# Optimization experiments

Hardware: AMD Instinct MI355X
Metric: run time of the kernel (lower is better)

The kernel has to match this reference:

```python
import jax, jax.numpy as jnp
import numpy as np

BN_EPS = 1e-5

def setup_inputs() -> dict:
    key = jax.random.key(0)
    k1, k2, k3, k4 = jax.random.split(key, 4)
    B, V, DI, DO = 4096, 64, 128, 128
    feat = jax.random.normal(k1, (B, V, DI), dtype=jnp.float32)
    adj = jax.random.uniform(k2, (V, V), dtype=jnp.float32)
    # per-vertex Linear weights (stacked): W[v] maps dim_in -> dim_out
    W = jax.random.normal(k3, (V, DI, DO), dtype=jnp.float32) * (1.0 / np.sqrt(DI))
    b = jax.random.normal(k4, (V, DO), dtype=jnp.float32) * 0.01
    gamma = jnp.ones((V, DO), dtype=jnp.float32)
    beta = jnp.zeros((V, DO), dtype=jnp.float32)
    return {"feat": feat, "adj": adj, "W": W, "b": b, "gamma": gamma, "beta": beta}

def reference(feat, adj, W, b, gamma, beta):
    # Per-vertex Linear as one grouped GEMM: [B,V,DI] x [V,DI,DO] -> [B,V,DO]
    h = jnp.einsum('bvi,vio->bvo', feat, W) + b[None, :, :]
    # BatchNorm1d (training mode): normalize over batch dim, per vertex & channel
    mu = jnp.mean(h, axis=0, keepdims=True)            # [1,V,DO]
    var = jnp.mean((h - mu) ** 2, axis=0, keepdims=True)  # biased variance
    h = (h - mu) * jax.lax.rsqrt(var + BN_EPS) * gamma[None] + beta[None]
    # adjacency mix: adj [V,V] applied to every batch element, then relu
    out = jnp.einsum('uv,bvo->buo', adj, h)
    return jax.nn.relu(out)
```

## Files before the change

### kernel.cpp

```cpp
#include <hip/hip_runtime.h>

#define BN 4096
#define VN 64
#define DI 128
#define DO 128

typedef __attribute__((ext_vector_type(8))) short short8;
typedef __attribute__((ext_vector_type(4))) float f32x4;

__device__ __forceinline__ float bf2f(unsigned short s) {
    return __uint_as_float(((unsigned)s) << 16);
}
__device__ __forceinline__ unsigned short f2bf(float f) {
    unsigned u = __float_as_uint(f);
    u += 0x7FFF + ((u >> 16) & 1);
    return (unsigned short)(u >> 16);
}
__device__ __forceinline__ unsigned pack_bf16_trunc(float lo, float hi) {
    return __builtin_amdgcn_perm(__float_as_uint(hi), __float_as_uint(lo), 0x07060302u);
}

__global__ __launch_bounds__(256) void k_prep(const float* __restrict__ W,
                                              const float* __restrict__ adj,
                                              unsigned short* __restrict__ Wt,
                                              unsigned short* __restrict__ adjbf,
                                              float* __restrict__ stats) {
    const int t = threadIdx.x, blk = blockIdx.x;
    if (blk < 256) {
        const int v = blk >> 2, q = blk & 3;
        const float* Wv = W + (size_t)v * DI * DO;
        unsigned short* Wtv = Wt + (size_t)v * DI * DO;
        const int o = t & 127;
        const int i0 = q * 32 + (t >> 7) * 16;
        short8 s0, s1;
#pragma unroll
        for (int j = 0; j < 8; ++j)
            s0[j] = (short)f2bf(Wv[(size_t)(i0 + j) * DO + o]);
#pragma unroll
        for (int j = 0; j < 8; ++j)
            s1[j] = (short)f2bf(Wv[(size_t)(i0 + 8 + j) * DO + o]);
        *(short8*)(Wtv + o * DI + i0) = s0;
        *(short8*)(Wtv + o * DI + i0 + 8) = s1;
    } else if (blk == 256) {
        short8 s0, s1;
#pragma unroll
        for (int j = 0; j < 8; ++j) s0[j] = (short)f2bf(adj[t * 16 + j]);
#pragma unroll
        for (int j = 0; j < 8; ++j) s1[j] = (short)f2bf(adj[t * 16 + 8 + j]);
        *(short8*)(adjbf + t * 16) = s0;
        *(short8*)(adjbf + t * 16 + 8) = s1;
    } else {
        const f32x4 z = {0.f, 0.f, 0.f, 0.f};
#pragma unroll
        for (int k = 0; k < 16; ++k)
            *(f32x4*)(stats + (size_t)(k * 256 + t) * 4) = z;
    }
}

__global__ __launch_bounds__(256) void k_gemm1(const float* __restrict__ feat,
                                               const unsigned short* __restrict__ Wt,
                                               const float* __restrict__ bias,
                                               unsigned short* __restrict__ h,
                                               float* __restrict__ sum_,
                                               float* __restrict__ sumsq_) {
    const int bt = blockIdx.x;
    const int v = blockIdx.y;
    const int tid = threadIdx.x;
    const int w = tid >> 6, lane = tid & 63;
    const int wm = w >> 1, wn = w & 1;
    const int quad = lane >> 4, l16 = lane & 15;

    size_t aidx[4];
    const unsigned short* Bbase[4];
#pragma unroll
    for (int rt = 0; rt < 4; ++rt)
        aidx[rt] = (size_t)(bt * 128 + wm * 64 + rt * 16 + l16) * (VN * DI)
                 + v * DI + quad * 8;
#pragma unroll
    for (int nt = 0; nt < 4; ++nt)
        Bbase[nt] = Wt + (size_t)v * (DI * DO)
                       + (size_t)(wn * 64 + nt * 16 + l16) * DI + quad * 8;

    f32x4 acc[4][4];
#pragma unroll
    for (int rt = 0; rt < 4; ++rt)
#pragma unroll
        for (int nt = 0; nt < 4; ++nt) acc[rt][nt] = (f32x4){0.f, 0.f, 0.f, 0.f};

#pragma unroll
    for (int k0 = 0; k0 < DI; k0 += 32) {
        short8 a[4], bb[4];
#pragma unroll
        for (int rt = 0; rt < 4; ++rt) {
            f32x4 f0 = *(const f32x4*)(feat + aidx[rt] + k0);
            f32x4 f1 = *(const f32x4*)(feat + aidx[rt] + k0 + 4);
            union { short8 s; unsigned u[4]; } pk;
            pk.u[0] = pack_bf16_trunc(f0[0], f0[1]);
            pk.u[1] = pack_bf16_trunc(f0[2], f0[3]);
            pk.u[2] = pack_bf16_trunc(f1[0], f1[1]);
            pk.u[3] = pack_bf16_trunc(f1[2], f1[3]);
            a[rt] = pk.s;
        }
#pragma unroll
        for (int nt = 0; nt < 4; ++nt) bb[nt] = *(const short8*)(Bbase[nt] + k0);
#pragma unroll
        for (int rt = 0; rt < 4; ++rt)
#pragma unroll
            for (int nt = 0; nt < 4; ++nt)
                acc[rt][nt] = __builtin_amdgcn_mfma_f32_16x16x32_bf16(
                    a[rt], bb[nt], acc[rt][nt], 0, 0, 0);
    }

#pragma unroll
    for (int nt = 0; nt < 4; ++nt) {
        const int col = wn * 64 + nt * 16 + l16;
        const float bv = bias[v * DO + col];
        float s = 0.f, sq = 0.f;
#pragma unroll
        for (int rt = 0; rt < 4; ++rt)
#pragma unroll
            for (int e = 0; e < 4; ++e) {
                float x = acc[rt][nt][e] + bv;
                acc[rt][nt][e] = x;
                s += x;
                sq += x * x;
            }
        s += __shfl_down(s, 32);  s += __shfl_down(s, 16);
        sq += __shfl_down(sq, 32); sq += __shfl_down(sq, 16);
        if (lane < 16) {
            atomicAdd(&sum_[v * DO + col], s);
            atomicAdd(&sumsq_[v * DO + col], sq);
        }
#pragma unroll
        for (int rt = 0; rt < 4; ++rt)
#pragma unroll
            for (int e = 0; e < 4; ++e) {
                int brow = bt * 128 + wm * 64 + rt * 16 + quad * 4 + e;
                h[(size_t)brow * (VN * DO) + v * DO + col] = f2bf(acc[rt][nt][e]);
            }
    }
}

__global__ __launch_bounds__(128) void k_stats(const float* __restrict__ sum_,
                                               const float* __restrict__ sumsq_,
                                               const float* __restrict__ adj,
                                               const float* __restrict__ gamma,
                                               const float* __restrict__ beta,
                                               float* __restrict__ scale,
                                               float* __restrict__ C0) {
    const int o = threadIdx.x;
    const int u = blockIdx.x;
    const float invB = 1.0f / (float)BN;
    if (u < VN) {
        float c0 = 0.f;
#pragma unroll
        for (int v = 0; v < VN; ++v) {
            float mu = sum_[v * DO + o] * invB;
            float var = sumsq_[v * DO + o] * invB - mu * mu;
            float inv = rsqrtf(var + 1e-5f);
            float sc = gamma[v * DO + o] * inv;
            c0 += adj[u * VN + v] * (beta[v * DO + o] - mu * sc);
        }
        C0[u * DO + o] = c0;
    } else {
#pragma unroll
        for (int v = 0; v < VN; ++v) {
            float mu = sum_[v * DO + o] * invB;
            float var = sumsq_[v * DO + o] * invB - mu * mu;
            scale[v * DO + o] = gamma[v * DO + o] * rsqrtf(var + 1e-5f);
        }
    }
}

__global__ __launch_bounds__(256) void k_mix(const unsigned short* __restrict__ h,
                                             const float* __restrict__ scale,
                                             const unsigned short* __restrict__ adjbf,
                                             const float* __restrict__ C0,
                                             float* __restrict__ out) {
    __shared__ unsigned short hsT[2][DO][72];
    const int t = threadIdx.x;
    const int b0 = blockIdx.x * 2;

    const int sv = t & 63;
#pragma unroll
    for (int c = 0; c < 8; ++c) {
        const int bl = c >> 2;
        const int o0 = ((t >> 6) << 3) + (c & 3) * 32;
        short8 hv = *(const short8*)(h + ((size_t)(b0 + bl) * VN + sv) * DO + o0);
        f32x4 s0 = *(const f32x4*)(scale + sv * DO + o0);
        f32x4 s1 = *(const f32x4*)(scale + sv * DO + o0 + 4);
#pragma unroll
        for (int j = 0; j < 4; ++j)
            hsT[bl][o0 + j][sv] = f2bf(bf2f((unsigned short)hv[j]) * s0[j]);
#pragma unroll
        for (int j = 0; j < 4; ++j)
            hsT[bl][o0 + 4 + j][sv] = f2bf(bf2f((unsigned short)hv[4 + j]) * s1[j]);
    }
    __syncthreads();

    const int w = t >> 6, lane = t & 63;
    const int bl = w >> 1, nh = w & 1;
    const int quad = lane >> 4, l16 = lane & 15;
    const int b = b0 + bl;

    short8 af[4][2];
#pragma unroll
    for (int mt = 0; mt < 4; ++mt)
#pragma unroll
        for (int ks = 0; ks < 2; ++ks)
            af[mt][ks] = *(const short8*)(adjbf + (mt * 16 + l16) * VN
                                          + ks * 32 + quad * 8);

    f32x4 acc[4][4];
#pragma unroll
    for (int mt = 0; mt < 4; ++mt)
#pragma unroll
        for (int nt = 0; nt < 4; ++nt) acc[mt][nt] = (f32x4){0.f, 0.f, 0.f, 0.f};

#pragma unroll
    for (int nt = 0; nt < 4; ++nt) {
        const unsigned short* bp = &hsT[bl][nh * 64 + nt * 16 + l16][quad * 8];
        short8 bf0 = *(const short8*)(bp);
        short8 bf1 = *(const short8*)(bp + 32);
#pragma unroll
        for (int mt = 0; mt < 4; ++mt) {
            acc[mt][nt] = __builtin_amdgcn_mfma_f32_16x16x32_bf16(
                af[mt][0], bf0, acc[mt][nt], 0, 0, 0);
            acc[mt][nt] = __builtin_amdgcn_mfma_f32_16x16x32_bf16(
                af[mt][1], bf1, acc[mt][nt], 0, 0, 0);
        }
    }

#pragma unroll
    for (int mt = 0; mt < 4; ++mt)
#pragma unroll
        for (int nt = 0; nt < 4; ++nt) {
            const int o = nh * 64 + nt * 16 + l16;
#pragma unroll
            for (int e = 0; e < 4; ++e) {
                const int u = mt * 16 + quad * 4 + e;
                out[((size_t)b * VN + u) * DO + o] =
                    fmaxf(acc[mt][nt][e] + C0[u * DO + o], 0.0f);
            }
        }
}

extern "C" void kernel_launch(void* const* d_in, const int* in_sizes, int n_in,
                              void* d_out, int out_size, void* d_ws, size_t ws_size,
                              hipStream_t stream) {
    const float* feat  = (const float*)d_in[0];
    const float* adj   = (const float*)d_in[1];
    const float* W     = (const float*)d_in[2];
    const float* bias  = (const float*)d_in[3];
    const float* gamma = (const float*)d_in[4];
    const float* beta  = (const float*)d_in[5];
    float* out = (float*)d_out;

    char* ws = (char*)d_ws;
    unsigned short* h     = (unsigned short*)ws;
    unsigned short* Wt    = (unsigned short*)(ws + 67108864ull);
    unsigned short* adjbf = (unsigned short*)(ws + 69206016ull);
    float* sum_   = (float*)(ws + 69214208ull);
    float* sumsq_ = sum_ + 8192;
    float* scale  = sumsq_ + 8192;
    float* C0     = scale + 8192;

    k_prep<<<dim3(258), dim3(256), 0, stream>>>(W, adj, Wt, adjbf, sum_);
    k_gemm1<<<dim3(32, 64), dim3(256), 0, stream>>>(feat, Wt, bias, h, sum_, sumsq_);
    k_stats<<<dim3(65), dim3(128), 0, stream>>>(sum_, sumsq_, adj, gamma, beta, scale, C0);
    k_mix<<<dim3(2048), dim3(256), 0, stream>>>(h, scale, adjbf, C0, out);
}
```

Baseline: 339.8 us.

## Replace BN stat atomics with partial sums, prefetch A tiles, preload W

BatchNorm sum and sum-of-squares atomics in the GEMM are replaced by per-block partial sums written to workspace. A new reduce kernel folds them into scale and shift, and a separate kernel computes the adjacency-mixed C0, so the stats zeroing pass is no longer needed. The GEMM now loads all W fragments into registers up front and double-buffers the feature loads across k-steps to overlap memory with MFMA. The prep kernel splits the W transpose across twice as many blocks. In exchange there is one extra kernel launch, and register pressure in the GEMM rises, which may lower occupancy.

```diff
diff --git a/kernel.cpp b/kernel.cpp
--- a/kernel.cpp
+++ b/kernel.cpp
@@ -23,25 +23,20 @@
 __global__ __launch_bounds__(256) void k_prep(const float* __restrict__ W,
                                               const float* __restrict__ adj,
                                               unsigned short* __restrict__ Wt,
-                                              unsigned short* __restrict__ adjbf,
-                                              float* __restrict__ stats) {
+                                              unsigned short* __restrict__ adjbf) {
     const int t = threadIdx.x, blk = blockIdx.x;
-    if (blk < 256) {
-        const int v = blk >> 2, q = blk & 3;
+    if (blk < 512) {
+        const int v = blk >> 3, q = blk & 7;
         const float* Wv = W + (size_t)v * DI * DO;
         unsigned short* Wtv = Wt + (size_t)v * DI * DO;
         const int o = t & 127;
-        const int i0 = q * 32 + (t >> 7) * 16;
-        short8 s0, s1;
+        const int i0 = q * 16 + (t >> 7) * 8;
+        short8 s0;
 #pragma unroll
         for (int j = 0; j < 8; ++j)
             s0[j] = (short)f2bf(Wv[(size_t)(i0 + j) * DO + o]);
-#pragma unroll
-        for (int j = 0; j < 8; ++j)
-            s1[j] = (short)f2bf(Wv[(size_t)(i0 + 8 + j) * DO + o]);
         *(short8*)(Wtv + o * DI + i0) = s0;
-        *(short8*)(Wtv + o * DI + i0 + 8) = s1;
-    } else if (blk == 256) {
+    } else {
         short8 s0, s1;
 #pragma unroll
         for (int j = 0; j < 8; ++j) s0[j] = (short)f2bf(adj[t * 16 + j]);
@@ -49,11 +44,6 @@
         for (int j = 0; j < 8; ++j) s1[j] = (short)f2bf(adj[t * 16 + 8 + j]);
         *(short8*)(adjbf + t * 16) = s0;
         *(short8*)(adjbf + t * 16 + 8) = s1;
-    } else {
-        const f32x4 z = {0.f, 0.f, 0.f, 0.f};
-#pragma unroll
-        for (int k = 0; k < 16; ++k)
-            *(f32x4*)(stats + (size_t)(k * 256 + t) * 4) = z;
     }
 }
 
@@ -61,8 +51,8 @@
                                                const unsigned short* __restrict__ Wt,
                                                const float* __restrict__ bias,
                                                unsigned short* __restrict__ h,
-                                               float* __restrict__ sum_,
-                                               float* __restrict__ sumsq_) {
+                                               float* __restrict__ psA,
+                                               float* __restrict__ psB) {
     const int bt = blockIdx.x;
     const int v = blockIdx.y;
     const int tid = threadIdx.x;
@@ -71,15 +61,19 @@
     const int quad = lane >> 4, l16 = lane & 15;
 
     size_t aidx[4];
-    const unsigned short* Bbase[4];
 #pragma unroll
     for (int rt = 0; rt < 4; ++rt)
         aidx[rt] = (size_t)(bt * 128 + wm * 64 + rt * 16 + l16) * (VN * DI)
                  + v * DI + quad * 8;
-#pragma unroll
-    for (int nt = 0; nt < 4; ++nt)
-        Bbase[nt] = Wt + (size_t)v * (DI * DO)
-                       + (size_t)(wn * 64 + nt * 16 + l16) * DI + quad * 8;
+
+    short8 bb[4][4];
+#pragma unroll
+    for (int ks = 0; ks < 4; ++ks)
+#pragma unroll
+        for (int nt = 0; nt < 4; ++nt)
+            bb[ks][nt] = *(const short8*)(Wt + (size_t)v * (DI * DO)
+                                          + (size_t)(wn * 64 + nt * 16 + l16) * DI
+                                          + quad * 8 + ks * 32);
 
     f32x4 acc[4][4];
 #pragma unroll
@@ -87,29 +81,35 @@
 #pragma unroll
         for (int nt = 0; nt < 4; ++nt) acc[rt][nt] = (f32x4){0.f, 0.f, 0.f, 0.f};
 
-#pragma unroll
-    for (int k0 = 0; k0 < DI; k0 += 32) {
-        short8 a[4], bb[4];
-#pragma unroll
-        for (int rt = 0; rt < 4; ++rt) {
-            f32x4 f0 = *(const f32x4*)(feat + aidx[rt] + k0);
-            f32x4 f1 = *(const f32x4*)(feat + aidx[rt] + k0 + 4);
-            union { short8 s; unsigned u[4]; } pk;
-            pk.u[0] = pack_bf16_trunc(f0[0], f0[1]);
-            pk.u[1] = pack_bf16_trunc(f0[2], f0[3]);
-            pk.u[2] = pack_bf16_trunc(f1[0], f1[1]);
-            pk.u[3] = pack_bf16_trunc(f1[2], f1[3]);
-            a[rt] = pk.s;
-        }
-#pragma unroll
-        for (int nt = 0; nt < 4; ++nt) bb[nt] = *(const short8*)(Bbase[nt] + k0);
+#define LOADA(dst, k0)                                                        \
+    {                                                                         \
+        _Pragma("unroll") for (int rt = 0; rt < 4; ++rt) {                    \
+            f32x4 f0 = *(const f32x4*)(feat + aidx[rt] + (k0));               \
+            f32x4 f1 = *(const f32x4*)(feat + aidx[rt] + (k0) + 4);          \
+            union { short8 s; unsigned u[4]; } pk;                            \
+            pk.u[0] = pack_bf16_trunc(f0[0], f0[1]);                          \
+            pk.u[1] = pack_bf16_trunc(f0[2], f0[3]);                          \
+            pk.u[2] = pack_bf16_trunc(f1[0], f1[1]);                          \
+            pk.u[3] = pack_bf16_trunc(f1[2], f1[3]);                          \
+            dst[rt] = pk.s;                                                   \
+        }                                                                     \
+    }
+
+    short8 aCur[4], aNxt[4];
+    LOADA(aCur, 0)
+#pragma unroll
+    for (int ks = 0; ks < 4; ++ks) {
+        if (ks < 3) LOADA(aNxt, (ks + 1) * 32)
 #pragma unroll
         for (int rt = 0; rt < 4; ++rt)
 #pragma unroll
             for (int nt = 0; nt < 4; ++nt)
                 acc[rt][nt] = __builtin_amdgcn_mfma_f32_16x16x32_bf16(
-                    a[rt], bb[nt], acc[rt][nt], 0, 0, 0);
-    }
+                    aCur[rt], bb[ks][nt], acc[rt][nt], 0, 0, 0);
+#pragma unroll
+        for (int rt = 0; rt < 4; ++rt) aCur[rt] = aNxt[rt];
+    }
+#undef LOADA
 
 #pragma unroll
     for (int nt = 0; nt < 4; ++nt) {
@@ -128,8 +128,9 @@
         s += __shfl_down(s, 32);  s += __shfl_down(s, 16);
         sq += __shfl_down(sq, 32); sq += __shfl_down(sq, 16);
         if (lane < 16) {
-            atomicAdd(&sum_[v * DO + col], s);
-            atomicAdd(&sumsq_[v * DO + col], sq);
+            const size_t pi = ((size_t)(v * 32 + bt) * 2 + wm) * 128 + col;
+            psA[pi] = s;
+            psB[pi] = sq;
         }
 #pragma unroll
         for (int rt = 0; rt < 4; ++rt)
@@ -141,35 +142,39 @@
     }
 }
 
-__global__ __launch_bounds__(128) void k_stats(const float* __restrict__ sum_,
-                                               const float* __restrict__ sumsq_,
-                                               const float* __restrict__ adj,
-                                               const float* __restrict__ gamma,
-                                               const float* __restrict__ beta,
-                                               float* __restrict__ scale,
-                                               float* __restrict__ C0) {
+__global__ __launch_bounds__(128) void k_reduce(const float* __restrict__ psA,
+                                                const float* __restrict__ psB,
+                                                const float* __restrict__ gamma,
+                                                const float* __restrict__ beta,
+                                                float* __restrict__ scale,
+                                                float* __restrict__ shift) {
+    const int o = threadIdx.x;
+    const int v = blockIdx.x;
+    float s = 0.f, sq = 0.f;
+#pragma unroll
+    for (int p = 0; p < 64; ++p) {
+        const size_t pi = ((size_t)v * 64 + p) * 128 + o;
+        s += psA[pi];
+        sq += psB[pi];
+    }
+    const float invB = 1.0f / (float)BN;
+    const float mu = s * invB;
+    const float var = sq * invB - mu * mu;
+    const float sc = gamma[v * DO + o] * rsqrtf(var + 1e-5f);
+    scale[v * DO + o] = sc;
+    shift[v * DO + o] = beta[v * DO + o] - mu * sc;
+}
+
+__global__ __launch_bounds__(128) void k_c0(const float* __restrict__ adj,
+                                            const float* __restrict__ shift,
+                                            float* __restrict__ C0) {
     const int o = threadIdx.x;
     const int u = blockIdx.x;
-    const float invB = 1.0f / (float)BN;
-    if (u < VN) {
-        float c0 = 0.f;
-#pragma unroll
-        for (int v = 0; v < VN; ++v) {
-            float mu = sum_[v * DO + o] * invB;
-            float var = sumsq_[v * DO + o] * invB - mu * mu;
-            float inv = rsqrtf(var + 1e-5f);
-            float sc = gamma[v * DO + o] * inv;
-            c0 += adj[u * VN + v] * (beta[v * DO + o] - mu * sc);
-        }
-        C0[u * DO + o] = c0;
-    } else {
-#pragma unroll
-        for (int v = 0; v < VN; ++v) {
-            float mu = sum_[v * DO + o] * invB;
-            float var = sumsq_[v * DO + o] * invB - mu * mu;
-            scale[v * DO + o] = gamma[v * DO + o] * rsqrtf(var + 1e-5f);
-        }
-    }
+    float c0 = 0.f;
+#pragma unroll
+    for (int v = 0; v < VN; ++v)
+        c0 += adj[u * VN + v] * shift[v * DO + o];
+    C0[u * DO + o] = c0;
 }
 
 __global__ __launch_bounds__(256) void k_mix(const unsigned short* __restrict__ h,
@@ -260,13 +265,15 @@
     unsigned short* h     = (unsigned short*)ws;
     unsigned short* Wt    = (unsigned short*)(ws + 67108864ull);
     unsigned short* adjbf = (unsigned short*)(ws + 69206016ull);
-    float* sum_   = (float*)(ws + 69214208ull);
-    float* sumsq_ = sum_ + 8192;
-    float* scale  = sumsq_ + 8192;
-    float* C0     = scale + 8192;
-
-    k_prep<<<dim3(258), dim3(256), 0, stream>>>(W, adj, Wt, adjbf, sum_);
-    k_gemm1<<<dim3(32, 64), dim3(256), 0, stream>>>(feat, Wt, bias, h, sum_, sumsq_);
-    k_stats<<<dim3(65), dim3(128), 0, stream>>>(sum_, sumsq_, adj, gamma, beta, scale, C0);
+    float* psA   = (float*)(ws + 69214208ull);
+    float* psB   = psA + 524288;
+    float* scale = psB + 524288;
+    float* shift = scale + 8192;
+    float* C0    = shift + 8192;
+
+    k_prep<<<dim3(513), dim3(256), 0, stream>>>(W, adj, Wt, adjbf);
+    k_gemm1<<<dim3(32, 64), dim3(256), 0, stream>>>(feat, Wt, bias, h, psA, psB);
+    k_reduce<<<dim3(64), dim3(128), 0, stream>>>(psA, psB, gamma, beta, scale, shift);
+    k_c0<<<dim3(64), dim3(128), 0, stream>>>(adj, shift, C0);
     k_mix<<<dim3(2048), dim3(256), 0, stream>>>(h, scale, adjbf, C0, out);
 }
```

Result: no change. 340.7 us (+0.3%).
